# Optimization experiments

Hardware: AMD Instinct MI355X
Metric: run time of the kernel (lower is better)

Reference implementation:

```python
import jax, jax.numpy as jnp
import numpy as np

TOP_K = 4


def setup_inputs() -> dict:
    key = jax.random.key(0)
    ks = jax.random.split(key, 5)
    B, T, D = 2, 1024, 1024
    P, PD = 256, 32  # n_patterns, pattern_dim
    return {
        "x": jax.random.normal(ks[0], (B, T, D), dtype=jnp.float32),
        "hasher_w": jax.random.normal(ks[1], (PD, D), dtype=jnp.float32) * 0.03,
        "keys": jax.random.normal(ks[2], (P, PD), dtype=jnp.float32) * 0.1,
        "values_down": jax.random.normal(ks[3], (P, D, PD), dtype=jnp.float32) * 0.01,
        "values_up": jax.random.normal(ks[4], (P, PD, D), dtype=jnp.float32) * 0.01,
        "scale": jnp.full((1,), 0.1, dtype=jnp.float32),
    }


def reference(x, hasher_w, keys, values_down, values_up, scale):
    # h = hasher(x): [B,T,pattern_dim]
    h = jnp.einsum("btd,pd->btp", x, hasher_w)
    # similarity to pattern keys: [B,T,n_patterns]
    sim = jnp.einsum("btp,np->btn", h, keys)
    vals, idx = jax.lax.top_k(sim, TOP_K)          # [B,T,TOP_K]
    w = jax.nn.softmax(vals, axis=-1)              # softmax over the top-k scores
    out = jnp.zeros_like(x)
    for k in range(TOP_K):  # small fixed loop, matches original
        ik = idx[..., k]                            # [B,T] int32
        vd = values_down[ik]                        # [B,T,D,PD] gathered per-token
        vu = values_up[ik]                          # [B,T,PD,D]
        proj = jax.nn.silu(jnp.einsum("btd,btdp->btp", x, vd))
        o = jnp.einsum("btp,btpd->btd", proj, vu)
        out = out + o * w[..., k:k + 1]
    return x + out * scale
```

## Files before the change

kernel.cpp:

```cpp
#include <hip/hip_runtime.h>
#include <math.h>
#include <float.h>

#define DDIM 1024
#define PDIM 32
#define NPAT 256
#define TOPK 4
#define BLOCK 256
#define GT   16
#define DCHP 128
#define NCHP 8
#define RTPB 4

__global__ __launch_bounds__(BLOCK) void route_kernel(
    const float* __restrict__ x,
    const float* __restrict__ hasher_w,
    const float* __restrict__ keys,
    int*   __restrict__ tki,
    float* __restrict__ tkw,
    int*   __restrict__ gcount,
    int ntok)
{
    __shared__ float shmem[RTPB * 64 * 33];
    __shared__ float h_s[RTPB][32];

    const int tid  = threadIdx.x;
    const int wv   = tid >> 6;
    const int lane = tid & 63;
    const int traw = blockIdx.x * RTPB + wv;
    const int tok  = min(traw, ntok - 1);

    const float4* xrow = (const float4*)(x + (size_t)tok * DDIM);
    float4 xr[4];
    #pragma unroll
    for (int i = 0; i < 4; ++i) xr[i] = xrow[i * 64 + lane];

    float part[PDIM];
    #pragma unroll
    for (int pp = 0; pp < PDIM; ++pp) part[pp] = 0.f;

    float* hs = shmem;
    for (int i = 0; i < 4; ++i) {
        #pragma unroll
        for (int k = 0; k < 8; ++k) {
            const int q  = k * 256 + tid;
            const int pp = q >> 6, fi = q & 63;
            ((float4*)hs)[q] =
                *(const float4*)(hasher_w + (size_t)pp * DDIM + i * 256 + fi * 4);
        }
        __syncthreads();
        #pragma unroll
        for (int pp = 0; pp < PDIM; ++pp) {
            const float4 w4 = *(const float4*)&hs[pp * 256 + lane * 4];
            part[pp] = fmaf(xr[i].x, w4.x, part[pp]);
            part[pp] = fmaf(xr[i].y, w4.y, part[pp]);
            part[pp] = fmaf(xr[i].z, w4.z, part[pp]);
            part[pp] = fmaf(xr[i].w, w4.w, part[pp]);
        }
        __syncthreads();
    }

    float* P = shmem + wv * (64 * 33);
    #pragma unroll
    for (int pp = 0; pp < PDIM; ++pp) P[lane * 33 + pp] = part[pp];
    __syncthreads();

    {
        const int pp = lane & 31, half = lane >> 5;
        float hsum = 0.f;
        #pragma unroll 8
        for (int i = 0; i < 32; ++i)
            hsum += P[(half * 32 + i) * 33 + pp];
        hsum += __shfl_xor(hsum, 32, 64);
        if (half == 0) h_s[wv][pp] = hsum;
    }
    __syncthreads();

    float4 h4[8];
    #pragma unroll
    for (int i = 0; i < 8; ++i) h4[i] = *(const float4*)&h_s[wv][i * 4];

    float sc0, sc1, sc2, sc3;
    {
        float sv[4];
        #pragma unroll
        for (int c = 0; c < 4; ++c) {
            const float4* kr = (const float4*)(keys + (size_t)(c * 64 + lane) * PDIM);
            float a = 0.f;
            #pragma unroll
            for (int i = 0; i < 8; ++i) {
                const float4 k4 = kr[i];
                a = fmaf(k4.x, h4[i].x, a); a = fmaf(k4.y, h4[i].y, a);
                a = fmaf(k4.z, h4[i].z, a); a = fmaf(k4.w, h4[i].w, a);
            }
            sv[c] = a;
        }
        sc0 = sv[0]; sc1 = sv[1]; sc2 = sv[2]; sc3 = sv[3];
    }

    float wval[TOPK]; int widx[TOPK];
    #pragma unroll
    for (int r = 0; r < TOPK; ++r) {
        float bv = sc0; int bc = 0;
        if (sc1 > bv) { bv = sc1; bc = 1; }
        if (sc2 > bv) { bv = sc2; bc = 2; }
        if (sc3 > bv) { bv = sc3; bc = 3; }
        int bidx = bc * 64 + lane;
        #pragma unroll
        for (int off = 1; off < 64; off <<= 1) {
            const float ov = __shfl_xor(bv, off, 64);
            const int   oi = __shfl_xor(bidx, off, 64);
            if (ov > bv || (ov == bv && oi < bidx)) { bv = ov; bidx = oi; }
        }
        wval[r] = bv; widx[r] = bidx;
        if ((bidx & 63) == lane) {
            const int c = bidx >> 6;
            if (c == 0) sc0 = -FLT_MAX;
            else if (c == 1) sc1 = -FLT_MAX;
            else if (c == 2) sc2 = -FLT_MAX;
            else sc3 = -FLT_MAX;
        }
    }

    if (lane == 0 && traw < ntok) {
        float m = wval[0];
        #pragma unroll
        for (int k = 1; k < TOPK; ++k) m = fmaxf(m, wval[k]);
        float s = 0.f, e[TOPK];
        #pragma unroll
        for (int k = 0; k < TOPK; ++k) { e[k] = expf(wval[k] - m); s += e[k]; }
        #pragma unroll
        for (int k = 0; k < TOPK; ++k) {
            tki[tok * TOPK + k] = widx[k];
            tkw[tok * TOPK + k] = e[k] / s;
            atomicAdd(&gcount[widx[k]], 1);
        }
    }
}

__global__ __launch_bounds__(NPAT) void scan_kernel(
    const int* __restrict__ gcount,
    int* __restrict__ offs,
    int* __restrict__ gcur,
    int* __restrict__ tile2p, int* __restrict__ tilei,
    int maxt)
{
    __shared__ int s[NPAT];
    const int tid = threadIdx.x;

    const int v = gcount[tid];
    s[tid] = v;
    __syncthreads();
    for (int off = 1; off < NPAT; off <<= 1) {
        int t = 0;
        if (tid >= off) t = s[tid - off];
        __syncthreads();
        s[tid] += t;
        __syncthreads();
    }
    const int incl = s[tid];
    offs[tid + 1] = incl;
    if (tid == 0) offs[0] = 0;
    gcur[tid] = incl - v;

    const int tc = (v + GT - 1) / GT;
    __syncthreads();
    s[tid] = tc;
    __syncthreads();
    for (int off = 1; off < NPAT; off <<= 1) {
        int t = 0;
        if (tid >= off) t = s[tid - off];
        __syncthreads();
        s[tid] += t;
        __syncthreads();
    }
    const int toff = s[tid] - tc;
    for (int i = tid; i < maxt; i += NPAT) tile2p[i] = -1;
    __syncthreads();
    for (int i = 0; i < tc; ++i) { tile2p[toff + i] = tid; tilei[toff + i] = i; }
}

__global__ __launch_bounds__(BLOCK) void fill_kernel(
    const int* __restrict__ tki, const float* __restrict__ tkw,
    const float* __restrict__ scale_p,
    int* __restrict__ gcur,
    int* __restrict__ etok, float* __restrict__ ew, int* __restrict__ slotof,
    int nent)
{
    const int e = blockIdx.x * BLOCK + threadIdx.x;
    if (e >= nent) return;
    const int p = tki[e];
    const int slot = atomicAdd(&gcur[p], 1);
    etok[slot] = e >> 2;
    ew[slot]   = tkw[e] * scale_p[0];
    slotof[e]  = slot;
}

__global__ __launch_bounds__(BLOCK, 6) void proj_kernel(
    const float* __restrict__ x,
    const float* __restrict__ vd,
    const int* __restrict__ offs,
    const int* __restrict__ etok,
    const int* __restrict__ tile2p,
    const int* __restrict__ tilei,
    float* __restrict__ part,
    int nent)
{
    __shared__ float vd_s[DCHP * PDIM];
    __shared__ float x_s[GT * DCHP];
    __shared__ int   gt[GT];
    __shared__ int   gs[GT];

    const int tb  = blockIdx.x >> 3;
    const int c   = blockIdx.x & 7;
    const int p   = tile2p[tb];
    if (p < 0) return;
    const int tid = threadIdx.x;
    const int off0 = offs[p] + tilei[tb] * GT;
    const int gv   = min(GT, offs[p + 1] - off0);

    const float* vdp = vd + (size_t)p * DDIM * PDIM + (size_t)c * DCHP * PDIM;
    #pragma unroll
    for (int k = 0; k < 4; ++k)
        ((float4*)vd_s)[k * 256 + tid] = ((const float4*)vdp)[k * 256 + tid];

    if (tid < GT) {
        if (tid < gv) { gt[tid] = etok[off0 + tid]; gs[tid] = off0 + tid; }
        else          { gt[tid] = etok[off0];       gs[tid] = nent; }
    }
    __syncthreads();

    #pragma unroll
    for (int k = 0; k < 2; ++k) {
        const int q  = k * 256 + tid;
        const int g  = q >> 5, fi = q & 31;
        ((float4*)x_s)[g * 32 + fi] =
            *(const float4*)(x + (size_t)gt[g] * DDIM + c * DCHP + fi * 4);
    }
    __syncthreads();

    const int lane = tid & 63;
    const int wv   = tid >> 6;
    const int pp4  = lane & 7;
    const int seg  = lane >> 3;

    float4 acc[4];
    #pragma unroll
    for (int j = 0; j < 4; ++j) acc[j] = make_float4(0.f, 0.f, 0.f, 0.f);

    #pragma unroll
    for (int i4 = 0; i4 < 4; ++i4) {
        const int d0 = seg * 16 + i4 * 4;
        const float4 v0 = *(const float4*)&vd_s[(d0 + 0) * PDIM + pp4 * 4];
        const float4 v1 = *(const float4*)&vd_s[(d0 + 1) * PDIM + pp4 * 4];
        const float4 v2 = *(const float4*)&vd_s[(d0 + 2) * PDIM + pp4 * 4];
        const float4 v3 = *(const float4*)&vd_s[(d0 + 3) * PDIM + pp4 * 4];
        #pragma unroll
        for (int j = 0; j < 4; ++j) {
            const float4 xg = *(const float4*)&x_s[(wv * 4 + j) * DCHP + d0];
            acc[j].x = fmaf(xg.x, v0.x, acc[j].x);
            acc[j].y = fmaf(xg.x, v0.y, acc[j].y);
            acc[j].z = fmaf(xg.x, v0.z, acc[j].z);
            acc[j].w = fmaf(xg.x, v0.w, acc[j].w);
            acc[j].x = fmaf(xg.y, v1.x, acc[j].x);
            acc[j].y = fmaf(xg.y, v1.y, acc[j].y);
            acc[j].z = fmaf(xg.y, v1.z, acc[j].z);
            acc[j].w = fmaf(xg.y, v1.w, acc[j].w);
            acc[j].x = fmaf(xg.z, v2.x, acc[j].x);
            acc[j].y = fmaf(xg.z, v2.y, acc[j].y);
            acc[j].z = fmaf(xg.z, v2.z, acc[j].z);
            acc[j].w = fmaf(xg.z, v2.w, acc[j].w);
            acc[j].x = fmaf(xg.w, v3.x, acc[j].x);
            acc[j].y = fmaf(xg.w, v3.y, acc[j].y);
            acc[j].z = fmaf(xg.w, v3.z, acc[j].z);
            acc[j].w = fmaf(xg.w, v3.w, acc[j].w);
        }
    }

    #pragma unroll
    for (int j = 0; j < 4; ++j) {
        #pragma unroll
        for (int off = 8; off <= 32; off <<= 1) {
            acc[j].x += __shfl_xor(acc[j].x, off, 64);
            acc[j].y += __shfl_xor(acc[j].y, off, 64);
            acc[j].z += __shfl_xor(acc[j].z, off, 64);
            acc[j].w += __shfl_xor(acc[j].w, off, 64);
        }
    }

    float* partc = part + (size_t)c * (size_t)(nent + 1) * PDIM;
    if ((lane & 0x38) == 0) {
        #pragma unroll
        for (int j = 0; j < 4; ++j)
            *(float4*)&partc[(size_t)gs[wv * 4 + j] * PDIM + pp4 * 4] = acc[j];
    }
}

template <int MODE>
__global__ __launch_bounds__(BLOCK, 6) void up_kernel(
    const float* __restrict__ vu,
    const int* __restrict__ offs,
    const int* __restrict__ etok,
    const float* __restrict__ ew,
    const int* __restrict__ tile2p,
    const int* __restrict__ tilei,
    const float* __restrict__ part,
    float* __restrict__ dst,
    int nent)
{
    __shared__ float vu_s[PDIM * DCHP];
    __shared__ float projT[PDIM][20];
    __shared__ int   gt[GT];
    __shared__ float gw[GT];
    __shared__ int   gs[GT];

    const int tb  = blockIdx.x >> 3;
    const int c   = blockIdx.x & 7;
    const int p   = tile2p[tb];
    if (p < 0) return;
    const int tid = threadIdx.x;
    const int off0 = offs[p] + tilei[tb] * GT;
    const int gv   = min(GT, offs[p + 1] - off0);

    const size_t PS = (size_t)(nent + 1) * PDIM;

    const float* vup = vu + (size_t)p * PDIM * DDIM + (size_t)c * DCHP;
    #pragma unroll
    for (int k = 0; k < 4; ++k) {
        const int q  = k * 256 + tid;
        const int pp = q >> 5, fi = q & 31;
        *(float4*)&vu_s[pp * DCHP + fi * 4] =
            *(const float4*)(vup + (size_t)pp * DDIM + fi * 4);
    }
    if (tid < GT) {
        if (tid < gv) {
            gt[tid] = etok[off0 + tid];
            gw[tid] = ew[off0 + tid];
            gs[tid] = off0 + tid;
        } else {
            gt[tid] = etok[off0]; gw[tid] = 0.f; gs[tid] = nent;
        }
    }
    __syncthreads();

    #pragma unroll
    for (int r = 0; r < 2; ++r) {
        const int idx = tid + r * BLOCK;
        const int g = idx >> 5, pp = idx & 31;
        const size_t row = (size_t)gs[g] * PDIM + pp;
        float s = 0.f;
        #pragma unroll
        for (int i = 0; i < NCHP; ++i) s += part[i * PS + row];
        const float pj = s / (1.f + expf(-s));
        projT[pp][g] = pj * gw[g];
    }
    __syncthreads();

    const int tg  = tid >> 5;
    const int l32 = tid & 31;
    const int g0 = tg * 2, g1 = tg * 2 + 1;

    float4 o0 = make_float4(0.f, 0.f, 0.f, 0.f);
    float4 o1 = o0;
    #pragma unroll
    for (int pp = 0; pp < PDIM; ++pp) {
        const float4 vu4 = *(const float4*)&vu_s[pp * DCHP + l32 * 4];
        const float a = projT[pp][g0];
        const float b = projT[pp][g1];
        o0.x = fmaf(a, vu4.x, o0.x); o0.y = fmaf(a, vu4.y, o0.y);
        o0.z = fmaf(a, vu4.z, o0.z); o0.w = fmaf(a, vu4.w, o0.w);
        o1.x = fmaf(b, vu4.x, o1.x); o1.y = fmaf(b, vu4.y, o1.y);
        o1.z = fmaf(b, vu4.z, o1.z); o1.w = fmaf(b, vu4.w, o1.w);
    }

    if (MODE == 0) {
        *(float4*)(dst + (size_t)gs[g0] * DDIM + c * DCHP + l32 * 4) = o0;
        *(float4*)(dst + (size_t)gs[g1] * DDIM + c * DCHP + l32 * 4) = o1;
    } else {
        if (g0 < gv) {
            float* op = dst + (size_t)gt[g0] * DDIM + c * DCHP + l32 * 4;
            atomicAdd(op + 0, o0.x); atomicAdd(op + 1, o0.y);
            atomicAdd(op + 2, o0.z); atomicAdd(op + 3, o0.w);
        }
        if (g1 < gv) {
            float* op = dst + (size_t)gt[g1] * DDIM + c * DCHP + l32 * 4;
            atomicAdd(op + 0, o1.x); atomicAdd(op + 1, o1.y);
            atomicAdd(op + 2, o1.z); atomicAdd(op + 3, o1.w);
        }
    }
}

__global__ __launch_bounds__(BLOCK) void combine_kernel(
    const float* __restrict__ x, const float* __restrict__ contrib,
    const int* __restrict__ slotof, float* __restrict__ out)
{
    __shared__ int sl[TOPK];
    const int t = blockIdx.x, tid = threadIdx.x;
    if (tid < TOPK) sl[tid] = slotof[t * TOPK + tid];
    __syncthreads();
    float4 r = ((const float4*)(x + (size_t)t * DDIM))[tid];
    #pragma unroll
    for (int k = 0; k < TOPK; ++k) {
        const float4 cv = ((const float4*)(contrib + (size_t)sl[k] * DDIM))[tid];
        r.x += cv.x; r.y += cv.y; r.z += cv.z; r.w += cv.w;
    }
    ((float4*)(out + (size_t)t * DDIM))[tid] = r;
}

extern "C" void kernel_launch(void* const* d_in, const int* in_sizes, int n_in,
                              void* d_out, int out_size, void* d_ws, size_t ws_size,
                              hipStream_t stream) {
    const float* x        = (const float*)d_in[0];
    const float* hasher_w = (const float*)d_in[1];
    const float* keys     = (const float*)d_in[2];
    const float* vd       = (const float*)d_in[3];
    const float* vu       = (const float*)d_in[4];
    const float* scale    = (const float*)d_in[5];
    float* out = (float*)d_out;

    const int ntok = in_sizes[0] / DDIM;
    if (ntok <= 0) return;
    const int nent = ntok * TOPK;
    const int maxt = (nent + GT - 1) / GT + NPAT;

    char* w = (char*)d_ws;
    const size_t o_gcnt = 0;
    const size_t o_gcur = 1024;
    const size_t o_offs = 2048;
    const size_t o_tki  = 4096;
    const size_t o_tkw  = o_tki  + (size_t)nent * 4;
    const size_t o_etok = o_tkw  + (size_t)nent * 4;
    const size_t o_ew   = o_etok + (size_t)nent * 4;
    const size_t o_slot = o_ew   + (size_t)nent * 4;
    const size_t o_t2p  = o_slot + (size_t)nent * 4;
    const size_t o_tli  = o_t2p  + (size_t)maxt * 4;
    const size_t o_part = (o_tli + (size_t)maxt * 4 + 255) & ~(size_t)255;
    const size_t partsz = (size_t)NCHP * (size_t)(nent + 1) * PDIM * 4;
    const size_t o_ctb  = (o_part + partsz + 255) & ~(size_t)255;
    const size_t needPart    = o_ctb;
    const size_t needContrib = o_ctb + (size_t)(nent + 1) * DDIM * 4;

    int*   gcount = (int*)(w + o_gcnt);
    int*   gcur   = (int*)(w + o_gcur);
    int*   offs   = (int*)(w + o_offs);
    int*   tki    = (int*)(w + o_tki);
    float* tkw    = (float*)(w + o_tkw);
    int*   etok   = (int*)(w + o_etok);
    float* ew     = (float*)(w + o_ew);
    int*   slotof = (int*)(w + o_slot);
    int*   tile2p = (int*)(w + o_t2p);
    int*   tilei  = (int*)(w + o_tli);
    float* part   = (float*)(w + o_part);
    float* contrib= (float*)(w + o_ctb);

    hipMemsetAsync(gcount, 0, NPAT * sizeof(int), stream);

    const int rblocks = (ntok + RTPB - 1) / RTPB;
    hipLaunchKernelGGL(route_kernel, dim3(rblocks), dim3(BLOCK), 0, stream,
                       x, hasher_w, keys, tki, tkw, gcount, ntok);
    hipLaunchKernelGGL(scan_kernel, dim3(1), dim3(NPAT), 0, stream,
                       gcount, offs, gcur, tile2p, tilei, maxt);
    hipLaunchKernelGGL(fill_kernel, dim3((nent + BLOCK - 1) / BLOCK), dim3(BLOCK),
                       0, stream, tki, tkw, scale, gcur, etok, ew, slotof, nent);
    hipLaunchKernelGGL(proj_kernel, dim3(maxt * NCHP), dim3(BLOCK), 0, stream,
                       x, vd, offs, etok, tile2p, tilei, part, nent);

    if (ws_size >= needContrib) {
        hipLaunchKernelGGL((up_kernel<0>), dim3(maxt * NCHP), dim3(BLOCK), 0, stream,
                           vu, offs, etok, ew, tile2p, tilei, part, contrib, nent);
        hipLaunchKernelGGL(combine_kernel, dim3(ntok), dim3(BLOCK), 0, stream,
                           x, contrib, slotof, out);
    } else if (ws_size >= needPart) {
        hipMemcpyAsync(out, x, (size_t)ntok * DDIM * 4, hipMemcpyDeviceToDevice,
                       stream);
        hipLaunchKernelGGL((up_kernel<1>), dim3(maxt * NCHP), dim3(BLOCK), 0, stream,
                           vu, offs, etok, ew, tile2p, tilei, part, out, nent);
    }
}
```

Measured before the change: 186.0 us.

## Route two tokens per wave and precompute SiLU-weighted projections once

The routing kernel now has each wavefront process two tokens, so every staged hasher weight tile in shared memory is reused twice and the number of route blocks is halved. A separate silu_kernel now sums the per-chunk partial projections, applies SiLU and the routing weight once per entry, and writes projW. The up kernel reads projW directly instead of redoing the 8-chunk reduction and exp in each of its 8 column-chunk blocks. This adds a kernel launch, a workspace buffer and more registers in the route kernel.

```diff
diff --git a/kernel.cpp b/kernel.cpp
--- a/kernel.cpp
+++ b/kernel.cpp
@@ -10,7 +10,7 @@
 #define GT   16
 #define DCHP 128
 #define NCHP 8
-#define RTPB 4
+#define RTPB 8
 
 __global__ __launch_bounds__(BLOCK) void route_kernel(
     const float* __restrict__ x,
@@ -21,23 +21,28 @@
     int*   __restrict__ gcount,
     int ntok)
 {
-    __shared__ float shmem[RTPB * 64 * 33];
-    __shared__ float h_s[RTPB][32];
+    __shared__ float shmem[4 * 64 * 33];
+    __shared__ float h_s[4][2][PDIM];
 
     const int tid  = threadIdx.x;
     const int wv   = tid >> 6;
     const int lane = tid & 63;
-    const int traw = blockIdx.x * RTPB + wv;
-    const int tok  = min(traw, ntok - 1);
-
-    const float4* xrow = (const float4*)(x + (size_t)tok * DDIM);
-    float4 xr[4];
-    #pragma unroll
-    for (int i = 0; i < 4; ++i) xr[i] = xrow[i * 64 + lane];
-
-    float part[PDIM];
-    #pragma unroll
-    for (int pp = 0; pp < PDIM; ++pp) part[pp] = 0.f;
+    const int traw0 = blockIdx.x * RTPB + wv * 2;
+    const int traw1 = traw0 + 1;
+    const int tok0 = min(traw0, ntok - 1);
+    const int tok1 = min(traw1, ntok - 1);
+
+    float4 xr0[4], xr1[4];
+    {
+        const float4* p0 = (const float4*)(x + (size_t)tok0 * DDIM);
+        const float4* p1 = (const float4*)(x + (size_t)tok1 * DDIM);
+        #pragma unroll
+        for (int i = 0; i < 4; ++i) { xr0[i] = p0[i * 64 + lane]; xr1[i] = p1[i * 64 + lane]; }
+    }
+
+    float part0[PDIM], part1[PDIM];
+    #pragma unroll
+    for (int pp = 0; pp < PDIM; ++pp) { part0[pp] = 0.f; part1[pp] = 0.f; }
 
     float* hs = shmem;
     for (int i = 0; i < 4; ++i) {
@@ -52,88 +57,101 @@
         #pragma unroll
         for (int pp = 0; pp < PDIM; ++pp) {
             const float4 w4 = *(const float4*)&hs[pp * 256 + lane * 4];
-            part[pp] = fmaf(xr[i].x, w4.x, part[pp]);
-            part[pp] = fmaf(xr[i].y, w4.y, part[pp]);
-            part[pp] = fmaf(xr[i].z, w4.z, part[pp]);
-            part[pp] = fmaf(xr[i].w, w4.w, part[pp]);
+            part0[pp] = fmaf(xr0[i].x, w4.x, part0[pp]);
+            part0[pp] = fmaf(xr0[i].y, w4.y, part0[pp]);
+            part0[pp] = fmaf(xr0[i].z, w4.z, part0[pp]);
+            part0[pp] = fmaf(xr0[i].w, w4.w, part0[pp]);
+            part1[pp] = fmaf(xr1[i].x, w4.x, part1[pp]);
+            part1[pp] = fmaf(xr1[i].y, w4.y, part1[pp]);
+            part1[pp] = fmaf(xr1[i].z, w4.z, part1[pp]);
+            part1[pp] = fmaf(xr1[i].w, w4.w, part1[pp]);
         }
         __syncthreads();
     }
 
     float* P = shmem + wv * (64 * 33);
     #pragma unroll
-    for (int pp = 0; pp < PDIM; ++pp) P[lane * 33 + pp] = part[pp];
-    __syncthreads();
-
-    {
-        const int pp = lane & 31, half = lane >> 5;
-        float hsum = 0.f;
-        #pragma unroll 8
-        for (int i = 0; i < 32; ++i)
-            hsum += P[(half * 32 + i) * 33 + pp];
-        hsum += __shfl_xor(hsum, 32, 64);
-        if (half == 0) h_s[wv][pp] = hsum;
-    }
-    __syncthreads();
-
-    float4 h4[8];
-    #pragma unroll
-    for (int i = 0; i < 8; ++i) h4[i] = *(const float4*)&h_s[wv][i * 4];
-
-    float sc0, sc1, sc2, sc3;
-    {
-        float sv[4];
-        #pragma unroll
-        for (int c = 0; c < 4; ++c) {
-            const float4* kr = (const float4*)(keys + (size_t)(c * 64 + lane) * PDIM);
-            float a = 0.f;
+    for (int t = 0; t < 2; ++t) {
+        const float* part = t ? part1 : part0;
+        #pragma unroll
+        for (int pp = 0; pp < PDIM; ++pp) P[lane * 33 + pp] = part[pp];
+        __syncthreads();
+        {
+            const int pp = lane & 31, half = lane >> 5;
+            float hsum = 0.f;
+            #pragma unroll 8
+            for (int i = 0; i < 32; ++i)
+                hsum += P[(half * 32 + i) * 33 + pp];
+            hsum += __shfl_xor(hsum, 32, 64);
+            if (half == 0) h_s[wv][t][pp] = hsum;
+        }
+        __syncthreads();
+    }
+
+    #pragma unroll
+    for (int t = 0; t < 2; ++t) {
+        const int traw = t ? traw1 : traw0;
+        const int tok  = t ? tok1  : tok0;
+
+        float4 h4[8];
+        #pragma unroll
+        for (int i = 0; i < 8; ++i) h4[i] = *(const float4*)&h_s[wv][t][i * 4];
+
+        float sc0, sc1, sc2, sc3;
+        {
+            float sv[4];
             #pragma unroll
-            for (int i = 0; i < 8; ++i) {
-                const float4 k4 = kr[i];
-                a = fmaf(k4.x, h4[i].x, a); a = fmaf(k4.y, h4[i].y, a);
-                a = fmaf(k4.z, h4[i].z, a); a = fmaf(k4.w, h4[i].w, a);
+            for (int c = 0; c < 4; ++c) {
+                const float4* kr = (const float4*)(keys + (size_t)(c * 64 + lane) * PDIM);
+                float a = 0.f;
+                #pragma unroll
+                for (int i = 0; i < 8; ++i) {
+                    const float4 k4 = kr[i];
+                    a = fmaf(k4.x, h4[i].x, a); a = fmaf(k4.y, h4[i].y, a);
+                    a = fmaf(k4.z, h4[i].z, a); a = fmaf(k4.w, h4[i].w, a);
+                }
+                sv[c] = a;
             }
-            sv[c] = a;
-        }
-        sc0 = sv[0]; sc1 = sv[1]; sc2 = sv[2]; sc3 = sv[3];
-    }
-
-    float wval[TOPK]; int widx[TOPK];
-    #pragma unroll
-    for (int r = 0; r < TOPK; ++r) {
-        float bv = sc0; int bc = 0;
-        if (sc1 > bv) { bv = sc1; bc = 1; }
-        if (sc2 > bv) { bv = sc2; bc = 2; }
-        if (sc3 > bv) { bv = sc3; bc = 3; }
-        int bidx = bc * 64 + lane;
-        #pragma unroll
-        for (int off = 1; off < 64; off <<= 1) {
-            const float ov = __shfl_xor(bv, off, 64);
-            const int   oi = __shfl_xor(bidx, off, 64);
-            if (ov > bv || (ov == bv && oi < bidx)) { bv = ov; bidx = oi; }
-        }
-        wval[r] = bv; widx[r] = bidx;
-        if ((bidx & 63) == lane) {
-            const int c = bidx >> 6;
-            if (c == 0) sc0 = -FLT_MAX;
-            else if (c == 1) sc1 = -FLT_MAX;
-            else if (c == 2) sc2 = -FLT_MAX;
-            else sc3 = -FLT_MAX;
-        }
-    }
-
-    if (lane == 0 && traw < ntok) {
-        float m = wval[0];
-        #pragma unroll
-        for (int k = 1; k < TOPK; ++k) m = fmaxf(m, wval[k]);
-        float s = 0.f, e[TOPK];
-        #pragma unroll
-        for (int k = 0; k < TOPK; ++k) { e[k] = expf(wval[k] - m); s += e[k]; }
-        #pragma unroll
-        for (int k = 0; k < TOPK; ++k) {
-            tki[tok * TOPK + k] = widx[k];
-            tkw[tok * TOPK + k] = e[k] / s;
-            atomicAdd(&gcount[widx[k]], 1);
+            sc0 = sv[0]; sc1 = sv[1]; sc2 = sv[2]; sc3 = sv[3];
+        }
+
+        float wval[TOPK]; int widx[TOPK];
+        #pragma unroll
+        for (int r = 0; r < TOPK; ++r) {
+            float bv = sc0; int bc = 0;
+            if (sc1 > bv) { bv = sc1; bc = 1; }
+            if (sc2 > bv) { bv = sc2; bc = 2; }
+            if (sc3 > bv) { bv = sc3; bc = 3; }
+            int bidx = bc * 64 + lane;
+            #pragma unroll
+            for (int off = 1; off < 64; off <<= 1) {
+                const float ov = __shfl_xor(bv, off, 64);
+                const int   oi = __shfl_xor(bidx, off, 64);
+                if (ov > bv || (ov == bv && oi < bidx)) { bv = ov; bidx = oi; }
+            }
+            wval[r] = bv; widx[r] = bidx;
+            if ((bidx & 63) == lane) {
+                const int c = bidx >> 6;
+                if (c == 0) sc0 = -FLT_MAX;
+                else if (c == 1) sc1 = -FLT_MAX;
+                else if (c == 2) sc2 = -FLT_MAX;
+                else sc3 = -FLT_MAX;
+            }
+        }
+
+        if (lane == 0 && traw < ntok) {
+            float m = wval[0];
+            #pragma unroll
+            for (int k = 1; k < TOPK; ++k) m = fmaxf(m, wval[k]);
+            float s = 0.f, e[TOPK];
+            #pragma unroll
+            for (int k = 0; k < TOPK; ++k) { e[k] = expf(wval[k] - m); s += e[k]; }
+            #pragma unroll
+            for (int k = 0; k < TOPK; ++k) {
+                tki[tok * TOPK + k] = widx[k];
+                tkw[tok * TOPK + k] = e[k] / s;
+                atomicAdd(&gcount[widx[k]], 1);
+            }
         }
     }
 }
@@ -296,22 +314,38 @@
     }
 }
 
+__global__ __launch_bounds__(BLOCK) void silu_kernel(
+    const float* __restrict__ part,
+    const float* __restrict__ ew,
+    float* __restrict__ projW,
+    int nent)
+{
+    const int idx = blockIdx.x * BLOCK + threadIdx.x;
+    const int total = (nent + 1) * PDIM;
+    if (idx >= total) return;
+    const int r = idx >> 5;
+    const size_t PS = (size_t)(nent + 1) * PDIM;
+    float s = 0.f;
+    #pragma unroll
+    for (int c = 0; c < NCHP; ++c) s += part[(size_t)c * PS + idx];
+    const float w = (r < nent) ? ew[r] : 0.f;
+    projW[idx] = (s / (1.f + expf(-s))) * w;
+}
+
 template <int MODE>
 __global__ __launch_bounds__(BLOCK, 6) void up_kernel(
     const float* __restrict__ vu,
     const int* __restrict__ offs,
     const int* __restrict__ etok,
-    const float* __restrict__ ew,
     const int* __restrict__ tile2p,
     const int* __restrict__ tilei,
-    const float* __restrict__ part,
+    const float* __restrict__ projW,
     float* __restrict__ dst,
     int nent)
 {
     __shared__ float vu_s[PDIM * DCHP];
     __shared__ float projT[PDIM][20];
     __shared__ int   gt[GT];
-    __shared__ float gw[GT];
     __shared__ int   gs[GT];
 
     const int tb  = blockIdx.x >> 3;
@@ -322,8 +356,6 @@
     const int off0 = offs[p] + tilei[tb] * GT;
     const int gv   = min(GT, offs[p + 1] - off0);
 
-    const size_t PS = (size_t)(nent + 1) * PDIM;
-
     const float* vup = vu + (size_t)p * PDIM * DDIM + (size_t)c * DCHP;
     #pragma unroll
     for (int k = 0; k < 4; ++k) {
@@ -333,13 +365,8 @@
             *(const float4*)(vup + (size_t)pp * DDIM + fi * 4);
     }
     if (tid < GT) {
-        if (tid < gv) {
-            gt[tid] = etok[off0 + tid];
-            gw[tid] = ew[off0 + tid];
-            gs[tid] = off0 + tid;
-        } else {
-            gt[tid] = etok[off0]; gw[tid] = 0.f; gs[tid] = nent;
-        }
+        if (tid < gv) { gt[tid] = etok[off0 + tid]; gs[tid] = off0 + tid; }
+        else          { gt[tid] = etok[off0];       gs[tid] = nent; }
     }
     __syncthreads();
 
@@ -347,12 +374,7 @@
     for (int r = 0; r < 2; ++r) {
         const int idx = tid + r * BLOCK;
         const int g = idx >> 5, pp = idx & 31;
-        const size_t row = (size_t)gs[g] * PDIM + pp;
-        float s = 0.f;
-        #pragma unroll
-        for (int i = 0; i < NCHP; ++i) s += part[i * PS + row];
-        const float pj = s / (1.f + expf(-s));
-        projT[pp][g] = pj * gw[g];
+        projT[pp][g] = projW[(size_t)gs[g] * PDIM + pp];
     }
     __syncthreads();
 
@@ -436,8 +458,10 @@
     const size_t o_tli  = o_t2p  + (size_t)maxt * 4;
     const size_t o_part = (o_tli + (size_t)maxt * 4 + 255) & ~(size_t)255;
     const size_t partsz = (size_t)NCHP * (size_t)(nent + 1) * PDIM * 4;
-    const size_t o_ctb  = (o_part + partsz + 255) & ~(size_t)255;
-    const size_t needPart    = o_ctb;
+    const size_t o_pw   = (o_part + partsz + 255) & ~(size_t)255;
+    const size_t pwsz   = (size_t)(nent + 1) * PDIM * 4;
+    const size_t o_ctb  = (o_pw + pwsz + 255) & ~(size_t)255;
+    const size_t needPW      = o_ctb;
     const size_t needContrib = o_ctb + (size_t)(nent + 1) * DDIM * 4;
 
     int*   gcount = (int*)(w + o_gcnt);
@@ -451,6 +475,7 @@
     int*   tile2p = (int*)(w + o_t2p);
     int*   tilei  = (int*)(w + o_tli);
     float* part   = (float*)(w + o_part);
+    float* projW  = (float*)(w + o_pw);
     float* contrib= (float*)(w + o_ctb);
 
     hipMemsetAsync(gcount, 0, NPAT * sizeof(int), stream);
@@ -462,18 +487,21 @@
                        gcount, offs, gcur, tile2p, tilei, maxt);
     hipLaunchKernelGGL(fill_kernel, dim3((nent + BLOCK - 1) / BLOCK), dim3(BLOCK),
                        0, stream, tki, tkw, scale, gcur, etok, ew, slotof, nent);
-    hipLaunchKernelGGL(proj_kernel, dim3(maxt * NCHP), dim3(BLOCK), 0, stream,
+    hipLaunchKernelGGL(proj_kernel, dim3(maxt * 8), dim3(BLOCK), 0, stream,
                        x, vd, offs, etok, tile2p, tilei, part, nent);
+    hipLaunchKernelGGL(silu_kernel,
+                       dim3(((nent + 1) * PDIM + BLOCK - 1) / BLOCK), dim3(BLOCK),
+                       0, stream, part, ew, projW, nent);
 
     if (ws_size >= needContrib) {
-        hipLaunchKernelGGL((up_kernel<0>), dim3(maxt * NCHP), dim3(BLOCK), 0, stream,
-                           vu, offs, etok, ew, tile2p, tilei, part, contrib, nent);
+        hipLaunchKernelGGL((up_kernel<0>), dim3(maxt * 8), dim3(BLOCK), 0, stream,
+                           vu, offs, etok, tile2p, tilei, projW, contrib, nent);
         hipLaunchKernelGGL(combine_kernel, dim3(ntok), dim3(BLOCK), 0, stream,
                            x, contrib, slotof, out);
-    } else if (ws_size >= needPart) {
+    } else if (ws_size >= needPW) {
         hipMemcpyAsync(out, x, (size_t)ntok * DDIM * 4, hipMemcpyDeviceToDevice,
                        stream);
-        hipLaunchKernelGGL((up_kernel<1>), dim3(maxt * NCHP), dim3(BLOCK), 0, stream,
-                           vu, offs, etok, ew, tile2p, tilei, part, out, nent);
-    }
-}
+        hipLaunchKernelGGL((up_kernel<1>), dim3(maxt * 8), dim3(BLOCK), 0, stream,
+                           vu, offs, etok, tile2p, tilei, projW, out, nent);
+    }
+}
```

Result: slower. 197.4 us (+6.2%).
